# Optimization experiments

Hardware: AMD Instinct MI355X
Metric: run time of the kernel (lower is better)

The kernel has to match this reference:

```python
import jax, jax.numpy as jnp
import numpy as np
import math

B, T, DIM = 4, 2048, 1024
N_HEADS, HEAD_DIM = 8, 128
WINDOW = 16
EPS = 1e-6
NEG = -1e9

def _alibi_slopes(n_heads):
    # n_heads=8 is a power of 2
    r = 2.0 ** (-8.0 / n_heads)
    return jnp.asarray([r ** i for i in range(n_heads)], dtype=jnp.float32)

def _rms_norm(x, w, eps):
    var = jnp.mean(jnp.square(x), axis=-1, keepdims=True)
    return x * jax.lax.rsqrt(var + eps) * w

def setup_inputs() -> dict:
    key = jax.random.key(0)
    ks = jax.random.split(key, 7)
    s = 1.0 / math.sqrt(DIM)
    return {
        "x": jax.random.normal(ks[0], (B, T, DIM), dtype=jnp.float32),
        # weights stored as [in, out]; apply as x @ W
        "wq": jax.random.normal(ks[1], (DIM, N_HEADS * HEAD_DIM), dtype=jnp.float32) * s,
        "wk": jax.random.normal(ks[2], (DIM, N_HEADS * HEAD_DIM), dtype=jnp.float32) * s,
        "wv": jax.random.normal(ks[3], (DIM, N_HEADS * HEAD_DIM), dtype=jnp.float32) * s,
        "wo": jax.random.normal(ks[4], (N_HEADS * HEAD_DIM, DIM), dtype=jnp.float32) * s,
        "q_norm_w": jnp.ones((N_HEADS * HEAD_DIM,), dtype=jnp.float32),
        "k_norm_w": jnp.ones((N_HEADS * HEAD_DIM,), dtype=jnp.float32),
    }

def reference(x, wq, wk, wv, wo, q_norm_w, k_norm_w):
    Bx, Tx, _ = x.shape
    xq = _rms_norm(x @ wq, q_norm_w, EPS)
    xk = _rms_norm(x @ wk, k_norm_w, EPS)
    xv = x @ wv
    # [B, H, T, D]
    q = xq.reshape(Bx, Tx, N_HEADS, HEAD_DIM).transpose(0, 2, 1, 3)
    k = xk.reshape(Bx, Tx, N_HEADS, HEAD_DIM).transpose(0, 2, 1, 3)
    v = xv.reshape(Bx, Tx, N_HEADS, HEAD_DIM).transpose(0, 2, 1, 3)

    pos = jnp.arange(Tx)
    rel = pos[None, :] - pos[:, None]            # rel[i, j] = j - i
    slopes = _alibi_slopes(N_HEADS)
    bias = slopes[:, None, None] * rel.astype(jnp.float32)  # [H, T, T]
    # causal (j > i) and sliding-window (j < i - WINDOW) masked
    invalid = (rel > 0) | (rel < -WINDOW)
    bias = jnp.where(invalid[None, :, :], NEG, bias)

    scale = 1.0 / math.sqrt(HEAD_DIM)
    scores = jnp.einsum("bhqd,bhkd->bhqk", q, k) * scale + bias[None]
    probs = jax.nn.softmax(scores, axis=-1)
    y = jnp.einsum("bhqk,bhkd->bhqd", probs, v)
    y = y.transpose(0, 2, 1, 3).reshape(Bx, Tx, N_HEADS * HEAD_DIM)
    return y @ wo
```

## Files before the change

### kernel.cpp

```cpp
#include <hip/hip_runtime.h>
#include <hip/hip_bf16.h>
#include <math.h>


#define TSEQ 2048
#define DIMW 1024
#define NHEAD 8
#define WIN 16

typedef __bf16 bf16x8_t __attribute__((ext_vector_type(8)));
typedef float f32x4_t __attribute__((ext_vector_type(4)));

__device__ __forceinline__ unsigned short f2bf(float f) {
  unsigned u = __float_as_uint(f);
  u += 0x7fffu + ((u >> 16) & 1u);
  return (unsigned short)(u >> 16);
}
__device__ __forceinline__ float bflo(unsigned u) { return __uint_as_float(u << 16); }
__device__ __forceinline__ float bfhi(unsigned u) { return __uint_as_float(u & 0xffff0000u); }

__global__ __launch_bounds__(256)
void k_conv_x(const float* __restrict__ x, unsigned short* __restrict__ xb, int n4) {
  int i = blockIdx.x * 256 + threadIdx.x;
  if (i >= n4) return;
  float4 v = ((const float4*)x)[i];
  ushort4 o;
  o.x = f2bf(v.x); o.y = f2bf(v.y); o.z = f2bf(v.z); o.w = f2bf(v.w);
  ((ushort4*)xb)[i] = o;
}

__global__ __launch_bounds__(256)
void k_conv_w(const float* __restrict__ wq, const float* __restrict__ wk,
              const float* __restrict__ wv, const float* __restrict__ wo,
              unsigned short* __restrict__ Wt) {
  __shared__ float tile[32][33];
  const int z = blockIdx.z;
  const float* src = (z == 0) ? wq : (z == 1) ? wk : (z == 2) ? wv : wo;
  const int n0 = blockIdx.x * 32;
  const int k0 = blockIdx.y * 32;
  const int tx = threadIdx.x, ty = threadIdx.y;
#pragma unroll
  for (int i = 0; i < 4; ++i)
    tile[ty + 8 * i][tx] = src[(size_t)(k0 + ty + 8 * i) * DIMW + n0 + tx];
  __syncthreads();
#pragma unroll
  for (int i = 0; i < 4; ++i)
    Wt[(size_t)z * DIMW * DIMW + (size_t)(n0 + ty + 8 * i) * DIMW + k0 + tx] =
        f2bf(tile[tx][ty + 8 * i]);
}

#define GLDS(gp, lp)                                                        \
  __builtin_amdgcn_global_load_lds(                                         \
      (const __attribute__((address_space(1))) void*)(gp),                  \
      (__attribute__((address_space(3))) void*)(lp), 16, 0, 0)

template <int MODE>
__global__ __launch_bounds__(512, 2)
void k_gemm(const unsigned short* __restrict__ A,
            const unsigned short* __restrict__ Bt,
            unsigned short* __restrict__ Cb,
            unsigned short* __restrict__ Vt,
            float* __restrict__ Cf,
            int M, int N, int K) {
  __shared__ __align__(16) unsigned char smem[98304];
  const int tid = threadIdx.x;
  const int lane = tid & 63;
  const int w = tid >> 6;
  const int wm = w >> 1, wn = w & 1;

  const int nwg = gridDim.x * gridDim.y;
  int flat = blockIdx.y * gridDim.x + blockIdx.x;
  flat = (flat & 7) * (nwg >> 3) + (flat >> 3);
  const int bx = flat % gridDim.x;
  const int by = flat / gridDim.x;

  const int r2 = lane >> 2;
  const int cg = ((lane & 3) ^ ((lane >> 3) & 3)) * 8;
  const size_t aS0 = (size_t)(by * 256 + w * 16 + r2) * K + cg;
  const size_t aS1 = aS0 + (size_t)128 * K;
  const size_t bS = (size_t)(bx * 128 + w * 16 + r2) * K + cg;
  const int dA0 = w * 1024;
  const int dA1 = 8192 + w * 1024;
  const int dB = 16384 + w * 1024;

  const int swz = ((lane >> 4) ^ ((lane >> 1) & 3)) * 16;
  const int aRd = (wm * 64 + (lane & 15)) * 64 + swz;
  const int bRd = 16384 + (wn * 64 + (lane & 15)) * 64 + swz;

  f32x4_t acc[4][4];
#pragma unroll
  for (int m = 0; m < 4; ++m)
#pragma unroll
    for (int n = 0; n < 4; ++n) acc[m][n] = (f32x4_t){0.f, 0.f, 0.f, 0.f};

  const int nc = K >> 5;
#pragma unroll
  for (int c = 0; c < 3; ++c) {
    unsigned char* s = smem + (c & 3) * 24576;
    GLDS(A + aS0 + c * 32, s + dA0);
    GLDS(A + aS1 + c * 32, s + dA1);
    GLDS(Bt + bS + c * 32, s + dB);
  }
#pragma unroll 1
  for (int c = 0; c < nc; ++c) {
    if (c + 2 < nc)      asm volatile("s_waitcnt vmcnt(6)" ::: "memory");
    else if (c + 1 < nc) asm volatile("s_waitcnt vmcnt(3)" ::: "memory");
    else                 asm volatile("s_waitcnt vmcnt(0)" ::: "memory");
    __builtin_amdgcn_s_barrier();
    unsigned char* s = smem + (c & 3) * 24576;
    if (c + 3 < nc) {
      unsigned char* sn = smem + ((c + 3) & 3) * 24576;
      GLDS(A + aS0 + (c + 3) * 32, sn + dA0);
      GLDS(A + aS1 + (c + 3) * 32, sn + dA1);
      GLDS(Bt + bS + (c + 3) * 32, sn + dB);
    }
    bf16x8_t af[4], bfr[4];
#pragma unroll
    for (int m = 0; m < 4; ++m) af[m] = *(const bf16x8_t*)(s + aRd + m * 1024);
#pragma unroll
    for (int n = 0; n < 4; ++n) bfr[n] = *(const bf16x8_t*)(s + bRd + n * 1024);
    __builtin_amdgcn_s_setprio(1);
#pragma unroll
    for (int m = 0; m < 4; ++m)
#pragma unroll
      for (int n = 0; n < 4; ++n)
        acc[m][n] = __builtin_amdgcn_mfma_f32_16x16x32_bf16(af[m], bfr[n], acc[m][n], 0, 0, 0);
    __builtin_amdgcn_s_setprio(0);
  }

  const int row0 = by * 256 + wm * 64 + ((lane >> 4) << 2);
  const int col0 = bx * 128 + wn * 64 + (lane & 15);
#pragma unroll
  for (int m = 0; m < 4; ++m)
#pragma unroll
    for (int n = 0; n < 4; ++n)
#pragma unroll
      for (int r = 0; r < 4; ++r) {
        const int row = row0 + m * 16 + r;
        const int col = col0 + n * 16;
        const float v = acc[m][n][r];
        if (MODE == 1) {
          Cf[(size_t)row * N + col] = v;
        } else if (col < 2048) {
          Cb[(size_t)row * 2048 + col] = f2bf(v);
        } else {
          const int vcol = col - 2048;
          const int hh = vcol >> 7, dd = vcol & 127;
          const int bb = row >> 11, tt = row & 2047;
          Vt[((size_t)(bb * NHEAD + hh) * 128 + dd) * TSEQ + tt] = f2bf(v);
        }
      }
}

__global__ __launch_bounds__(256)
void k_rmsnorm(unsigned short* __restrict__ qk, const float* __restrict__ qw,
               const float* __restrict__ kw) {
  const int row = blockIdx.x;
  const int tid = threadIdx.x;
  unsigned short* base = qk + (size_t)row * 2048;
  uint2 uq = *(const uint2*)(base + tid * 4);
  uint2 uk = *(const uint2*)(base + 1024 + tid * 4);
  float q0 = bflo(uq.x), q1 = bfhi(uq.x), q2 = bflo(uq.y), q3 = bfhi(uq.y);
  float k0 = bflo(uk.x), k1 = bfhi(uk.x), k2 = bflo(uk.y), k3 = bfhi(uk.y);
  float sq = q0 * q0 + q1 * q1 + q2 * q2 + q3 * q3;
  float sk = k0 * k0 + k1 * k1 + k2 * k2 + k3 * k3;
#pragma unroll
  for (int off = 32; off > 0; off >>= 1) {
    sq += __shfl_xor(sq, off);
    sk += __shfl_xor(sk, off);
  }
  __shared__ float red[8];
  const int w = tid >> 6;
  if ((tid & 63) == 0) { red[w] = sq; red[4 + w] = sk; }
  __syncthreads();
  sq = red[0] + red[1] + red[2] + red[3];
  sk = red[4] + red[5] + red[6] + red[7];
  const float rq = rsqrtf(sq * (1.0f / 1024.0f) + 1e-6f);
  const float rk = rsqrtf(sk * (1.0f / 1024.0f) + 1e-6f);
  const int c = tid * 4;
  uint2 oq, ok;
  oq.x = (unsigned)f2bf(q0 * rq * qw[c]) | ((unsigned)f2bf(q1 * rq * qw[c + 1]) << 16);
  oq.y = (unsigned)f2bf(q2 * rq * qw[c + 2]) | ((unsigned)f2bf(q3 * rq * qw[c + 3]) << 16);
  ok.x = (unsigned)f2bf(k0 * rk * kw[c]) | ((unsigned)f2bf(k1 * rk * kw[c + 1]) << 16);
  ok.y = (unsigned)f2bf(k2 * rk * kw[c + 2]) | ((unsigned)f2bf(k3 * rk * kw[c + 3]) << 16);
  *(uint2*)(base + tid * 4) = oq;
  *(uint2*)(base + 1024 + tid * 4) = ok;
}

__global__ __launch_bounds__(256)
void k_attn(const unsigned short* __restrict__ qk,
            const unsigned short* __restrict__ vt,
            unsigned short* __restrict__ outb) {
  __shared__ __align__(16) unsigned char plds_all[4][1280];
  const int lane = threadIdx.x & 63;
  const int wv = threadIdx.x >> 6;
  unsigned char* plds = plds_all[wv];
  const int bh = blockIdx.y;
  const int b = bh >> 3, h = bh & 7;
  const int t0 = blockIdx.x * 64 + wv * 16;
  const int g = lane >> 4, c = lane & 15;
  const int jlo = t0 - 16;

  const unsigned short* qrow = qk + (size_t)(b * TSEQ + t0 + c) * 2048 + h * 128 + g * 8;
  bf16x8_t qf[4];
#pragma unroll
  for (int kc = 0; kc < 4; ++kc) qf[kc] = *(const bf16x8_t*)(qrow + kc * 32);

  const int j0 = jlo + c;
  const int j0c = (j0 < 0) ? 0 : j0;
  const unsigned short* krow0 = qk + (size_t)(b * TSEQ + j0c) * 2048 + 1024 + h * 128 + g * 8;
  const unsigned short* krow1 = qk + (size_t)(b * TSEQ + t0 + c) * 2048 + 1024 + h * 128 + g * 8;
  bf16x8_t kf0[4], kf1[4];
#pragma unroll
  for (int kc = 0; kc < 4; ++kc) {
    kf0[kc] = *(const bf16x8_t*)(krow0 + kc * 32);
    kf1[kc] = *(const bf16x8_t*)(krow1 + kc * 32);
  }

  f32x4_t s0 = (f32x4_t){0.f, 0.f, 0.f, 0.f};
  f32x4_t s1 = (f32x4_t){0.f, 0.f, 0.f, 0.f};
#pragma unroll
  for (int kc = 0; kc < 4; ++kc) {
    s0 = __builtin_amdgcn_mfma_f32_16x16x32_bf16(kf0[kc], qf[kc], s0, 0, 0, 0);
    s1 = __builtin_amdgcn_mfma_f32_16x16x32_bf16(kf1[kc], qf[kc], s1, 0, 0, 0);
  }

  const float scale = 0.08838834764831845f;
  const float slope = 1.0f / (float)(1 << h);
  float val[8];
#pragma unroll
  for (int z = 0; z < 2; ++z)
#pragma unroll
    for (int r = 0; r < 4; ++r) {
      const int kk = z * 16 + g * 4 + r;
      const int rel = kk - 16 - c;
      const bool ok = (rel <= 0) & (rel >= -WIN) & (jlo + kk >= 0);
      const float sc = (z == 0) ? s0[r] : s1[r];
      val[z * 4 + r] = ok ? (sc * scale + slope * (float)rel) : -1.0e30f;
    }
  float m = val[0];
#pragma unroll
  for (int i = 1; i < 8; ++i) m = fmaxf(m, val[i]);
  m = fmaxf(m, __shfl_xor(m, 16));
  m = fmaxf(m, __shfl_xor(m, 32));
  float e[8], s = 0.f;
#pragma unroll
  for (int i = 0; i < 8; ++i) { e[i] = __expf(val[i] - m); s += e[i]; }
  s += __shfl_xor(s, 16);
  s += __shfl_xor(s, 32);
  const float inv = 1.0f / s;

#pragma unroll
  for (int z = 0; z < 2; ++z) {
    uint2 pk;
    pk.x = (unsigned)f2bf(e[z * 4 + 0] * inv) | ((unsigned)f2bf(e[z * 4 + 1] * inv) << 16);
    pk.y = (unsigned)f2bf(e[z * 4 + 2] * inv) | ((unsigned)f2bf(e[z * 4 + 3] * inv) << 16);
    *(uint2*)(plds + c * 80 + z * 32 + g * 8) = pk;
  }
  const bf16x8_t pf = *(const bf16x8_t*)(plds + c * 80 + g * 16);

  const int vc0 = jlo + g * 8;
  const int vcc = (vc0 < 0) ? 0 : vc0;
  const unsigned short* vbase = vt + (size_t)(bh * 128 + c) * TSEQ + vcc;
  unsigned short* orow = outb + (size_t)(b * TSEQ + t0) * 1024 + h * 128 + c;
#pragma unroll
  for (int n = 0; n < 8; ++n) {
    const bf16x8_t vf = *(const bf16x8_t*)(vbase + (size_t)n * 16 * TSEQ);
    f32x4_t o = __builtin_amdgcn_mfma_f32_16x16x32_bf16(pf, vf, (f32x4_t){0.f, 0.f, 0.f, 0.f},
                                                        0, 0, 0);
#pragma unroll
    for (int r = 0; r < 4; ++r)
      orow[(size_t)(g * 4 + r) * 1024 + n * 16] = f2bf(o[r]);
  }
}

extern "C" void kernel_launch(void* const* d_in, const int* in_sizes, int n_in,
                              void* d_out, int out_size, void* d_ws, size_t ws_size,
                              hipStream_t stream) {
  const float* x = (const float*)d_in[0];
  const float* wq = (const float*)d_in[1];
  const float* wk = (const float*)d_in[2];
  const float* wv = (const float*)d_in[3];
  const float* wo = (const float*)d_in[4];
  const float* qnw = (const float*)d_in[5];
  const float* knw = (const float*)d_in[6];
  float* out = (float*)d_out;

  const int M = 4 * TSEQ;
  unsigned short* xb = (unsigned short*)d_ws;
  unsigned short* Wt = xb + (size_t)M * DIMW;
  unsigned short* qkb = Wt + (size_t)4 * DIMW * DIMW;
  unsigned short* Vt = qkb + (size_t)M * 2048;
  if (ws_size < ((size_t)M * DIMW + (size_t)4 * DIMW * DIMW + (size_t)M * 2048 +
                 (size_t)M * 2048) * 2) return;

  k_conv_x<<<(M * DIMW / 4 + 255) / 256, 256, 0, stream>>>(x, xb, M * DIMW / 4);
  k_conv_w<<<dim3(32, 32, 4), dim3(32, 8), 0, stream>>>(wq, wk, wv, wo, Wt);
  k_gemm<0><<<dim3(24, 32), 512, 0, stream>>>(xb, Wt, qkb, Vt, nullptr, M, 3072, 1024);
  k_rmsnorm<<<M, 256, 0, stream>>>(qkb, qnw, knw);
  k_attn<<<dim3(TSEQ / 64, 32), 256, 0, stream>>>(qkb, Vt, xb);
  k_gemm<1><<<dim3(8, 32), 512, 0, stream>>>(xb, Wt + (size_t)3 * DIMW * DIMW, nullptr,
                                             nullptr, out, M, 1024, 1024);
}
```

Measured before the change: 235.6 us.

## Restructure bf16 GEMM with larger tiles and two-stage K-64 pipelining

Templates the GEMM on tile width, using 256x256 tiles for the QKV projection and 256x128 for the output projection. Warps move to a 2x4 layout, each owning 128 rows. The K loop becomes 64-wide double-buffered stages, each split into two 32-wide halves, with the async LDS loads interleaved between MFMA phases. The epilogue branch is hoisted per block. The aim is more operand reuse per LDS byte and fewer barriers per MFMA. The costs are much larger accumulator and LDS footprints: 128 KB of LDS and 256 accumulator floats for BN=256. Under the (512,2) launch bounds this risks register spills or lower occupancy.

```diff
diff --git a/kernel.cpp b/kernel.cpp
--- a/kernel.cpp
+++ b/kernel.cpp
@@ -54,7 +54,9 @@
       (const __attribute__((address_space(1))) void*)(gp),                  \
       (__attribute__((address_space(3))) void*)(lp), 16, 0, 0)
 
-template <int MODE>
+#define BAR asm volatile("s_barrier" ::: "memory")
+
+template <int MODE, int BN>
 __global__ __launch_bounds__(512, 2)
 void k_gemm(const unsigned short* __restrict__ A,
             const unsigned short* __restrict__ Bt,
@@ -62,11 +64,15 @@
             unsigned short* __restrict__ Vt,
             float* __restrict__ Cf,
             int M, int N, int K) {
-  __shared__ __align__(16) unsigned char smem[98304];
+  constexpr int WN = BN / 4;
+  constexpr int NF = WN / 16;
+  constexpr int BSLICE = BN * 64;
+  constexpr int HALF = 32768 + BN * 128;
+  __shared__ __align__(16) unsigned char smem[2 * HALF];
   const int tid = threadIdx.x;
   const int lane = tid & 63;
   const int w = tid >> 6;
-  const int wm = w >> 1, wn = w & 1;
+  const int wm = w >> 2, wn = w & 3;
 
   const int nwg = gridDim.x * gridDim.y;
   int flat = blockIdx.y * gridDim.x + blockIdx.x;
@@ -76,80 +82,119 @@
 
   const int r2 = lane >> 2;
   const int cg = ((lane & 3) ^ ((lane >> 3) & 3)) * 8;
-  const size_t aS0 = (size_t)(by * 256 + w * 16 + r2) * K + cg;
-  const size_t aS1 = aS0 + (size_t)128 * K;
-  const size_t bS = (size_t)(bx * 128 + w * 16 + r2) * K + cg;
-  const int dA0 = w * 1024;
-  const int dA1 = 8192 + w * 1024;
-  const int dB = 16384 + w * 1024;
+
+#define IA(q_, kt_, s_, h_)                                                      \
+  GLDS(A + (size_t)(by * 256 + (h_)*128 + w * 16 + r2) * K + (kt_)*64 + (s_)*32 + cg, \
+       smem + (q_)*HALF + (s_)*16384 + ((h_)*128 + w * 16) * 64)
+#define IB(q_, kt_, s_, h_)                                                      \
+  GLDS(Bt + (size_t)(bx * BN + (h_)*128 + w * 16 + r2) * K + (kt_)*64 + (s_)*32 + cg, \
+       smem + (q_)*HALF + 32768 + (s_)*BSLICE + ((h_)*128 + w * 16) * 64)
 
   const int swz = ((lane >> 4) ^ ((lane >> 1) & 3)) * 16;
-  const int aRd = (wm * 64 + (lane & 15)) * 64 + swz;
-  const int bRd = 16384 + (wn * 64 + (lane & 15)) * 64 + swz;
-
-  f32x4_t acc[4][4];
-#pragma unroll
-  for (int m = 0; m < 4; ++m)
-#pragma unroll
-    for (int n = 0; n < 4; ++n) acc[m][n] = (f32x4_t){0.f, 0.f, 0.f, 0.f};
-
-  const int nc = K >> 5;
-#pragma unroll
-  for (int c = 0; c < 3; ++c) {
-    unsigned char* s = smem + (c & 3) * 24576;
-    GLDS(A + aS0 + c * 32, s + dA0);
-    GLDS(A + aS1 + c * 32, s + dA1);
-    GLDS(Bt + bS + c * 32, s + dB);
+  const int aBase = (wm * 128 + (lane & 15)) * 64 + swz;
+  const int bBase = 32768 + (wn * WN + (lane & 15)) * 64 + swz;
+
+  f32x4_t acc[8][NF];
+#pragma unroll
+  for (int m = 0; m < 8; ++m)
+#pragma unroll
+    for (int n = 0; n < NF; ++n) acc[m][n] = (f32x4_t){0.f, 0.f, 0.f, 0.f};
+  bf16x8_t af[4], bfr[NF];
+  const unsigned char* bp;
+
+#define PHASE(s_, mq_, DO_B)                                                     \
+  {                                                                              \
+    _Pragma("unroll") for (int m = 0; m < 4; ++m)                                \
+        af[m] = *(const bf16x8_t*)(bp + (s_)*16384 + aBase + ((mq_)*4 + m) * 1024); \
+    if (DO_B) {                                                                  \
+      _Pragma("unroll") for (int n = 0; n < NF; ++n)                             \
+          bfr[n] = *(const bf16x8_t*)(bp + (s_)*BSLICE + bBase + n * 1024);      \
+    }                                                                            \
+    __builtin_amdgcn_s_setprio(1);                                               \
+    _Pragma("unroll") for (int m = 0; m < 4; ++m)                                \
+        _Pragma("unroll") for (int n = 0; n < NF; ++n)                           \
+            acc[(mq_)*4 + m][n] = __builtin_amdgcn_mfma_f32_16x16x32_bf16(       \
+                af[m], bfr[n], acc[(mq_)*4 + m][n], 0, 0, 0);                    \
+    __builtin_amdgcn_s_setprio(0);                                               \
+  }
+#define VMC_S                                                                    \
+  do {                                                                           \
+    if (BN == 256) asm volatile("s_waitcnt vmcnt(4)" ::: "memory");              \
+    else           asm volatile("s_waitcnt vmcnt(3)" ::: "memory");              \
+  } while (0)
+
+  const int nt = K >> 6;
+  if (BN == 256) {
+    IA(0, 0, 0, 0); IB(0, 0, 0, 0); IB(0, 0, 0, 1); IA(0, 0, 0, 1);
+    IA(0, 0, 1, 0); IB(0, 0, 1, 0); IB(0, 0, 1, 1); IA(0, 0, 1, 1);
+  } else {
+    IA(0, 0, 0, 0); IB(0, 0, 0, 0); IA(0, 0, 0, 1);
+    IA(0, 0, 1, 0); IB(0, 0, 1, 0); IA(0, 0, 1, 1);
   }
 #pragma unroll 1
-  for (int c = 0; c < nc; ++c) {
-    if (c + 2 < nc)      asm volatile("s_waitcnt vmcnt(6)" ::: "memory");
-    else if (c + 1 < nc) asm volatile("s_waitcnt vmcnt(3)" ::: "memory");
-    else                 asm volatile("s_waitcnt vmcnt(0)" ::: "memory");
-    __builtin_amdgcn_s_barrier();
-    unsigned char* s = smem + (c & 3) * 24576;
-    if (c + 3 < nc) {
-      unsigned char* sn = smem + ((c + 3) & 3) * 24576;
-      GLDS(A + aS0 + (c + 3) * 32, sn + dA0);
-      GLDS(A + aS1 + (c + 3) * 32, sn + dA1);
-      GLDS(Bt + bS + (c + 3) * 32, sn + dB);
-    }
-    bf16x8_t af[4], bfr[4];
-#pragma unroll
-    for (int m = 0; m < 4; ++m) af[m] = *(const bf16x8_t*)(s + aRd + m * 1024);
-#pragma unroll
-    for (int n = 0; n < 4; ++n) bfr[n] = *(const bf16x8_t*)(s + bRd + n * 1024);
-    __builtin_amdgcn_s_setprio(1);
-#pragma unroll
-    for (int m = 0; m < 4; ++m)
-#pragma unroll
-      for (int n = 0; n < 4; ++n)
-        acc[m][n] = __builtin_amdgcn_mfma_f32_16x16x32_bf16(af[m], bfr[n], acc[m][n], 0, 0, 0);
-    __builtin_amdgcn_s_setprio(0);
-  }
-
-  const int row0 = by * 256 + wm * 64 + ((lane >> 4) << 2);
-  const int col0 = bx * 128 + wn * 64 + (lane & 15);
-#pragma unroll
-  for (int m = 0; m < 4; ++m)
-#pragma unroll
-    for (int n = 0; n < 4; ++n)
-#pragma unroll
-      for (int r = 0; r < 4; ++r) {
-        const int row = row0 + m * 16 + r;
-        const int col = col0 + n * 16;
-        const float v = acc[m][n][r];
-        if (MODE == 1) {
-          Cf[(size_t)row * N + col] = v;
-        } else if (col < 2048) {
-          Cb[(size_t)row * 2048 + col] = f2bf(v);
-        } else {
-          const int vcol = col - 2048;
+  for (int t = 0; t < nt - 1; ++t) {
+    const int p = t & 1, q = p ^ 1;
+    const int kn = t + 1;
+    bp = smem + p * HALF;
+    VMC_S; BAR;
+    IA(q, kn, 0, 0); IB(q, kn, 0, 0);
+    PHASE(0, 0, true);
+    if (BN == 256) { IB(q, kn, 0, 1); IA(q, kn, 0, 1); }
+    else           { IA(q, kn, 0, 1); }
+    PHASE(0, 1, false);
+    VMC_S; BAR;
+    IA(q, kn, 1, 0); IB(q, kn, 1, 0);
+    PHASE(1, 0, true);
+    if (BN == 256) { IB(q, kn, 1, 1); IA(q, kn, 1, 1); }
+    else           { IA(q, kn, 1, 1); }
+    PHASE(1, 1, false);
+  }
+  {
+    bp = smem + ((nt - 1) & 1) * HALF;
+    VMC_S; BAR;
+    PHASE(0, 0, true);
+    PHASE(0, 1, false);
+    asm volatile("s_waitcnt vmcnt(0)" ::: "memory"); BAR;
+    PHASE(1, 0, true);
+    PHASE(1, 1, false);
+  }
+
+  const int row0 = by * 256 + wm * 128 + ((lane >> 4) << 2);
+  const int col0 = bx * BN + wn * WN + (lane & 15);
+  if (MODE == 1) {
+#pragma unroll
+    for (int m = 0; m < 8; ++m)
+#pragma unroll
+      for (int n = 0; n < NF; ++n)
+#pragma unroll
+        for (int r = 0; r < 4; ++r)
+          Cf[(size_t)(row0 + m * 16 + r) * N + col0 + n * 16] = acc[m][n][r];
+  } else if (bx * BN < 2048) {
+#pragma unroll
+    for (int m = 0; m < 8; ++m)
+#pragma unroll
+      for (int n = 0; n < NF; ++n)
+#pragma unroll
+        for (int r = 0; r < 4; ++r)
+          Cb[(size_t)(row0 + m * 16 + r) * 2048 + col0 + n * 16] = f2bf(acc[m][n][r]);
+  } else {
+#pragma unroll
+    for (int m = 0; m < 8; ++m)
+#pragma unroll
+      for (int n = 0; n < NF; ++n)
+#pragma unroll
+        for (int r = 0; r < 4; ++r) {
+          const int row = row0 + m * 16 + r;
+          const int vcol = col0 + n * 16 - 2048;
           const int hh = vcol >> 7, dd = vcol & 127;
           const int bb = row >> 11, tt = row & 2047;
-          Vt[((size_t)(bb * NHEAD + hh) * 128 + dd) * TSEQ + tt] = f2bf(v);
+          Vt[((size_t)(bb * NHEAD + hh) * 128 + dd) * TSEQ + tt] = f2bf(acc[m][n][r]);
         }
-      }
+  }
+#undef IA
+#undef IB
+#undef PHASE
+#undef VMC_S
 }
 
 __global__ __launch_bounds__(256)
@@ -296,9 +341,9 @@
 
   k_conv_x<<<(M * DIMW / 4 + 255) / 256, 256, 0, stream>>>(x, xb, M * DIMW / 4);
   k_conv_w<<<dim3(32, 32, 4), dim3(32, 8), 0, stream>>>(wq, wk, wv, wo, Wt);
-  k_gemm<0><<<dim3(24, 32), 512, 0, stream>>>(xb, Wt, qkb, Vt, nullptr, M, 3072, 1024);
+  k_gemm<0, 256><<<dim3(12, 32), 512, 0, stream>>>(xb, Wt, qkb, Vt, nullptr, M, 3072, 1024);
   k_rmsnorm<<<M, 256, 0, stream>>>(qkb, qnw, knw);
   k_attn<<<dim3(TSEQ / 64, 32), 256, 0, stream>>>(qkb, Vt, xb);
-  k_gemm<1><<<dim3(8, 32), 512, 0, stream>>>(xb, Wt + (size_t)3 * DIMW * DIMW, nullptr,
-                                             nullptr, out, M, 1024, 1024);
-}
+  k_gemm<1, 128><<<dim3(8, 32), 512, 0, stream>>>(xb, Wt + (size_t)3 * DIMW * DIMW, nullptr,
+                                                  nullptr, out, M, 1024, 1024);
+}
```

Measured after the change: 216.5 us. -8.1%, faster.

## Shrink GEMM tiles to 128x128 with triple buffering and block V layout for attention

Applied to the files above, without the earlier changes.

The GEMM goes from 256x128 tiles with 512 threads and a 4-slot LDS ring to 128x128 tiles with 256 threads, a 3-slot ring and 48KB of LDS. This doubles the grid and allows more resident blocks per CU. The epilogue branches once per block instead of once per element, and V is stored in a [bh][t/8][d][8] blocked layout. The attention kernel now loads all V fragments as contiguous 16-byte chunks early, overlapping them with the QK MFMAs. The cost is less reuse per tile, so global and LDS traffic per FLOP goes up.

```diff
diff --git a/kernel.cpp b/kernel.cpp
--- a/kernel.cpp
+++ b/kernel.cpp
@@ -55,14 +55,14 @@
       (__attribute__((address_space(3))) void*)(lp), 16, 0, 0)
 
 template <int MODE>
-__global__ __launch_bounds__(512, 2)
+__global__ __launch_bounds__(256, 3)
 void k_gemm(const unsigned short* __restrict__ A,
             const unsigned short* __restrict__ Bt,
             unsigned short* __restrict__ Cb,
             unsigned short* __restrict__ Vt,
             float* __restrict__ Cf,
             int M, int N, int K) {
-  __shared__ __align__(16) unsigned char smem[98304];
+  __shared__ __align__(16) unsigned char smem[49152];
   const int tid = threadIdx.x;
   const int lane = tid & 63;
   const int w = tid >> 6;
@@ -76,16 +76,23 @@
 
   const int r2 = lane >> 2;
   const int cg = ((lane & 3) ^ ((lane >> 3) & 3)) * 8;
-  const size_t aS0 = (size_t)(by * 256 + w * 16 + r2) * K + cg;
-  const size_t aS1 = aS0 + (size_t)128 * K;
-  const size_t bS = (size_t)(bx * 128 + w * 16 + r2) * K + cg;
-  const int dA0 = w * 1024;
-  const int dA1 = 8192 + w * 1024;
-  const int dB = 16384 + w * 1024;
+
+#define IA(sl_, ks_, h_)                                                       \
+  GLDS(A + (size_t)(by * 128 + (h_)*64 + w * 16 + r2) * K + (ks_)*32 + cg,     \
+       smem + (sl_)*16384 + ((h_)*64 + w * 16) * 64)
+#define IB(sl_, ks_, h_)                                                       \
+  GLDS(Bt + (size_t)(bx * 128 + (h_)*64 + w * 16 + r2) * K + (ks_)*32 + cg,    \
+       smem + (sl_)*16384 + 8192 + ((h_)*64 + w * 16) * 64)
+#define STAGE(ks_)                                                             \
+  do {                                                                         \
+    const int sl_ = (ks_) % 3;                                                 \
+    IA(sl_, (ks_), 0); IB(sl_, (ks_), 0);                                      \
+    IA(sl_, (ks_), 1); IB(sl_, (ks_), 1);                                      \
+  } while (0)
 
   const int swz = ((lane >> 4) ^ ((lane >> 1) & 3)) * 16;
   const int aRd = (wm * 64 + (lane & 15)) * 64 + swz;
-  const int bRd = 16384 + (wn * 64 + (lane & 15)) * 64 + swz;
+  const int bRd = 8192 + (wn * 64 + (lane & 15)) * 64 + swz;
 
   f32x4_t acc[4][4];
 #pragma unroll
@@ -93,32 +100,20 @@
 #pragma unroll
     for (int n = 0; n < 4; ++n) acc[m][n] = (f32x4_t){0.f, 0.f, 0.f, 0.f};
 
-  const int nc = K >> 5;
-#pragma unroll
-  for (int c = 0; c < 3; ++c) {
-    unsigned char* s = smem + (c & 3) * 24576;
-    GLDS(A + aS0 + c * 32, s + dA0);
-    GLDS(A + aS1 + c * 32, s + dA1);
-    GLDS(Bt + bS + c * 32, s + dB);
-  }
+  const int NS = K >> 5;
+  STAGE(0); STAGE(1);
 #pragma unroll 1
-  for (int c = 0; c < nc; ++c) {
-    if (c + 2 < nc)      asm volatile("s_waitcnt vmcnt(6)" ::: "memory");
-    else if (c + 1 < nc) asm volatile("s_waitcnt vmcnt(3)" ::: "memory");
-    else                 asm volatile("s_waitcnt vmcnt(0)" ::: "memory");
-    __builtin_amdgcn_s_barrier();
-    unsigned char* s = smem + (c & 3) * 24576;
-    if (c + 3 < nc) {
-      unsigned char* sn = smem + ((c + 3) & 3) * 24576;
-      GLDS(A + aS0 + (c + 3) * 32, sn + dA0);
-      GLDS(A + aS1 + (c + 3) * 32, sn + dA1);
-      GLDS(Bt + bS + (c + 3) * 32, sn + dB);
-    }
+  for (int s = 0; s < NS; ++s) {
+    if (s + 1 < NS) asm volatile("s_waitcnt vmcnt(4)" ::: "memory");
+    else            asm volatile("s_waitcnt vmcnt(0)" ::: "memory");
+    asm volatile("s_barrier" ::: "memory");
+    if (s + 2 < NS) STAGE(s + 2);
+    const unsigned char* sp = smem + (s % 3) * 16384;
     bf16x8_t af[4], bfr[4];
 #pragma unroll
-    for (int m = 0; m < 4; ++m) af[m] = *(const bf16x8_t*)(s + aRd + m * 1024);
-#pragma unroll
-    for (int n = 0; n < 4; ++n) bfr[n] = *(const bf16x8_t*)(s + bRd + n * 1024);
+    for (int n = 0; n < 4; ++n) bfr[n] = *(const bf16x8_t*)(sp + bRd + n * 1024);
+#pragma unroll
+    for (int m = 0; m < 4; ++m) af[m] = *(const bf16x8_t*)(sp + aRd + m * 1024);
     __builtin_amdgcn_s_setprio(1);
 #pragma unroll
     for (int m = 0; m < 4; ++m)
@@ -128,28 +123,42 @@
     __builtin_amdgcn_s_setprio(0);
   }
 
-  const int row0 = by * 256 + wm * 64 + ((lane >> 4) << 2);
+  const int row0 = by * 128 + wm * 64 + ((lane >> 4) << 2);
   const int col0 = bx * 128 + wn * 64 + (lane & 15);
-#pragma unroll
-  for (int m = 0; m < 4; ++m)
-#pragma unroll
-    for (int n = 0; n < 4; ++n)
-#pragma unroll
-      for (int r = 0; r < 4; ++r) {
-        const int row = row0 + m * 16 + r;
-        const int col = col0 + n * 16;
-        const float v = acc[m][n][r];
-        if (MODE == 1) {
-          Cf[(size_t)row * N + col] = v;
-        } else if (col < 2048) {
-          Cb[(size_t)row * 2048 + col] = f2bf(v);
-        } else {
-          const int vcol = col - 2048;
+  if (MODE == 1) {
+#pragma unroll
+    for (int m = 0; m < 4; ++m)
+#pragma unroll
+      for (int n = 0; n < 4; ++n)
+#pragma unroll
+        for (int r = 0; r < 4; ++r)
+          Cf[(size_t)(row0 + m * 16 + r) * N + col0 + n * 16] = acc[m][n][r];
+  } else if (bx * 128 < 2048) {
+#pragma unroll
+    for (int m = 0; m < 4; ++m)
+#pragma unroll
+      for (int n = 0; n < 4; ++n)
+#pragma unroll
+        for (int r = 0; r < 4; ++r)
+          Cb[(size_t)(row0 + m * 16 + r) * 2048 + col0 + n * 16] = f2bf(acc[m][n][r]);
+  } else {
+#pragma unroll
+    for (int m = 0; m < 4; ++m)
+#pragma unroll
+      for (int n = 0; n < 4; ++n)
+#pragma unroll
+        for (int r = 0; r < 4; ++r) {
+          const int row = row0 + m * 16 + r;
+          const int vcol = col0 + n * 16 - 2048;
           const int hh = vcol >> 7, dd = vcol & 127;
           const int bb = row >> 11, tt = row & 2047;
-          Vt[((size_t)(bb * NHEAD + hh) * 128 + dd) * TSEQ + tt] = f2bf(v);
+          Vt[((((size_t)(bb * NHEAD + hh)) * 256 + (tt >> 3)) * 128 + dd) * 8 + (tt & 7)] =
+              f2bf(acc[m][n][r]);
         }
-      }
+  }
+#undef IA
+#undef IB
+#undef STAGE
 }
 
 __global__ __launch_bounds__(256)
@@ -217,6 +226,13 @@
     kf1[kc] = *(const bf16x8_t*)(krow1 + kc * 32);
   }
 
+  int tc = (jlo >> 3) + g;
+  if (tc < 0) tc = 0;
+  const unsigned short* vbase = vt + (((size_t)bh * 256 + tc) * 128 + c) * 8;
+  bf16x8_t vf[8];
+#pragma unroll
+  for (int n = 0; n < 8; ++n) vf[n] = *(const bf16x8_t*)(vbase + n * 128);
+
   f32x4_t s0 = (f32x4_t){0.f, 0.f, 0.f, 0.f};
   f32x4_t s1 = (f32x4_t){0.f, 0.f, 0.f, 0.f};
 #pragma unroll
@@ -259,14 +275,10 @@
   }
   const bf16x8_t pf = *(const bf16x8_t*)(plds + c * 80 + g * 16);
 
-  const int vc0 = jlo + g * 8;
-  const int vcc = (vc0 < 0) ? 0 : vc0;
-  const unsigned short* vbase = vt + (size_t)(bh * 128 + c) * TSEQ + vcc;
   unsigned short* orow = outb + (size_t)(b * TSEQ + t0) * 1024 + h * 128 + c;
 #pragma unroll
   for (int n = 0; n < 8; ++n) {
-    const bf16x8_t vf = *(const bf16x8_t*)(vbase + (size_t)n * 16 * TSEQ);
-    f32x4_t o = __builtin_amdgcn_mfma_f32_16x16x32_bf16(pf, vf, (f32x4_t){0.f, 0.f, 0.f, 0.f},
+    f32x4_t o = __builtin_amdgcn_mfma_f32_16x16x32_bf16(pf, vf[n], (f32x4_t){0.f, 0.f, 0.f, 0.f},
                                                         0, 0, 0);
 #pragma unroll
     for (int r = 0; r < 4; ++r)
@@ -296,9 +308,9 @@
 
   k_conv_x<<<(M * DIMW / 4 + 255) / 256, 256, 0, stream>>>(x, xb, M * DIMW / 4);
   k_conv_w<<<dim3(32, 32, 4), dim3(32, 8), 0, stream>>>(wq, wk, wv, wo, Wt);
-  k_gemm<0><<<dim3(24, 32), 512, 0, stream>>>(xb, Wt, qkb, Vt, nullptr, M, 3072, 1024);
+  k_gemm<0><<<dim3(24, 64), 256, 0, stream>>>(xb, Wt, qkb, Vt, nullptr, M, 3072, 1024);
   k_rmsnorm<<<M, 256, 0, stream>>>(qkb, qnw, knw);
   k_attn<<<dim3(TSEQ / 64, 32), 256, 0, stream>>>(qkb, Vt, xb);
-  k_gemm<1><<<dim3(8, 32), 512, 0, stream>>>(xb, Wt + (size_t)3 * DIMW * DIMW, nullptr,
+  k_gemm<1><<<dim3(8, 64), 256, 0, stream>>>(xb, Wt + (size_t)3 * DIMW * DIMW, nullptr,
                                              nullptr, out, M, 1024, 1024);
 }
```

After: 215.5 us. 8.5% less time.
